# Performance work log

Hardware: AMD Instinct MI355X
Metric: run time of the kernel (lower is better)

Reference implementation:

```python
import jax, jax.numpy as jnp
import numpy as np

N_NODES = 100000
N_EDGES = 1600000
N_GRAPHS = 1024
IN_FEATS = 74
HID = 100


def setup_inputs() -> dict:
    key = jax.random.key(0)
    ks = jax.random.split(key, 16)
    node_feats = jax.random.normal(ks[0], (N_NODES, IN_FEATS), dtype=jnp.float32)
    src = jax.random.randint(ks[1], (N_EDGES,), 0, N_NODES, dtype=jnp.int32)
    dst = jax.random.randint(ks[2], (N_EDGES,), 0, N_NODES, dtype=jnp.int32)
    graph_ids = jnp.sort(jax.random.randint(ks[3], (N_NODES,), 0, N_GRAPHS, dtype=jnp.int32))

    def lin(k, fi, fo):
        s = 1.0 / np.sqrt(fi)
        kw, kb = jax.random.split(k)
        return (jax.random.uniform(kw, (fi, fo), jnp.float32, -s, s),
                jax.random.uniform(kb, (fo,), jnp.float32, -s, s))

    W_self1, _ = lin(ks[4], IN_FEATS, HID)
    W_neigh1, b1 = lin(ks[5], IN_FEATS, HID)
    W_self2, _ = lin(ks[6], HID, HID)
    W_neigh2, b2 = lin(ks[7], HID, HID)
    w_atom, b_atom = lin(ks[8], HID, 1)
    W_p1, b_p1 = lin(ks[9], 2 * HID, 64)
    W_p2, b_p2 = lin(ks[10], 64, 1)
    return {
        'node_feats': node_feats, 'src': src, 'dst': dst, 'graph_ids': graph_ids,
        'n_graphs': N_GRAPHS,
        'W_self1': W_self1, 'W_neigh1': W_neigh1, 'b1': b1,
        'W_self2': W_self2, 'W_neigh2': W_neigh2, 'b2': b2,
        'w_atom': w_atom, 'b_atom': b_atom,
        'W_p1': W_p1, 'b_p1': b_p1, 'W_p2': W_p2, 'b_p2': b_p2,
    }


def _sage_mean_layer(h, src, dst, W_self, W_neigh, b):
    # DGL SAGEConv, aggregator 'mean': out = h @ W_self + mean_{u->v}(h_u) @ W_neigh + b
    n = h.shape[0]
    msg = h[src]  # [E, F] gather
    agg = jax.ops.segment_sum(msg, dst, num_segments=n)
    deg = jax.ops.segment_sum(jnp.ones((src.shape[0],), h.dtype), dst, num_segments=n)
    h_neigh = agg / jnp.maximum(deg, 1.0)[:, None]
    return jax.nn.relu(h @ W_self + h_neigh @ W_neigh + b)


def reference(node_feats, src, dst, graph_ids, n_graphs,
              W_self1, W_neigh1, b1, W_self2, W_neigh2, b2,
              w_atom, b_atom, W_p1, b_p1, W_p2, b_p2):
    h = _sage_mean_layer(node_feats, src, dst, W_self1, W_neigh1, b1)
    h = _sage_mean_layer(h, src, dst, W_self2, W_neigh2, b2)

    # WeightedSumAndMax readout
    w = jax.nn.sigmoid(h @ w_atom + b_atom)          # [N, 1]
    g_sum = jax.ops.segment_sum(h * w, graph_ids, num_segments=n_graphs)   # [G, HID]
    g_max = jax.ops.segment_max(h, graph_ids, num_segments=n_graphs)       # [G, HID]
    g_max = jnp.where(jnp.isneginf(g_max), 0.0, g_max)  # empty graphs -> 0
    g_feats = jnp.concatenate([g_sum, g_max], axis=-1)  # [G, 2*HID]

    # MLP predictor: Linear(200,64) -> Linear(64,1) (no activation between)
    out = (g_feats @ W_p1 + b_p1) @ W_p2 + b_p2
    return out
```

## Files before the change

kernel.cpp:

```cpp
#include <hip/hip_runtime.h>

#define N_NODES 100000
#define N_PAD   100096
#define N_EDGES 1600000
#define N_GRAPHS 1024
#define F_IN 74
#define HID 100

#define KP1 160
#define KP2 224

#define FBF_LD 80
#define F8T_LD 80
#define AGT_LD 80
#define AGT2_LD 112
#define H1C8_LD 128
#define H2_LD  100

#define ZROW N_NODES

#define NB ((N_NODES + 255) / 256)
#define BKCAP 8192
#define BIN_EPB 4096
#define NBB ((N_EDGES + BIN_EPB - 1) / BIN_EPB)

typedef __attribute__((ext_vector_type(8))) short short8;
typedef __attribute__((ext_vector_type(4))) float f32x4;
typedef __attribute__((ext_vector_type(2))) float f32x2;

#if defined(__has_builtin)
#if __has_builtin(__builtin_amdgcn_cvt_pk_f32_fp8) && __has_builtin(__builtin_amdgcn_cvt_pk_fp8_f32)
#define HAVE_FP8 1
#endif
#endif

__device__ __forceinline__ unsigned short f2bf(float x) {
    union { float f; unsigned u; } c; c.f = x;
    unsigned u = c.u;
    unsigned r = (u + 0x7fffu + ((u >> 16) & 1u)) >> 16;
    return (unsigned short)r;
}
__device__ __forceinline__ float bf2f(unsigned short h) {
    union { unsigned u; float f; } c; c.u = ((unsigned)h) << 16;
    return c.f;
}
__device__ __forceinline__ float blo(unsigned w) { return bf2f((unsigned short)(w & 0xffffu)); }
__device__ __forceinline__ float bhi(unsigned w) { return bf2f((unsigned short)(w >> 16)); }
__device__ __forceinline__ unsigned bpack(float a, float b) {
    return (unsigned)f2bf(a) | ((unsigned)f2bf(b) << 16);
}
__device__ __forceinline__ void store8(void* p, unsigned lo, unsigned hi) {
    unsigned long long v = (unsigned long long)lo | ((unsigned long long)hi << 32);
    *(unsigned long long*)p = v;
}

__device__ __forceinline__ unsigned char enc_fp8_1(float v) {
#ifdef HAVE_FP8
    return (unsigned char)__builtin_amdgcn_cvt_pk_fp8_f32(v, 0.f, 0, false);
#else
    unsigned sgn = v < 0.f ? 0x80u : 0u;
    float m = fabsf(v);
    unsigned char mag;
    if (m < 0.015625f) {
        int q = (int)(m * 512.0f + 0.5f);
        mag = (unsigned char)(q > 7 ? 7 : q);
    } else {
        union { float f; unsigned u; } c; c.f = m;
        unsigned r = c.u + 0x7ffff + ((c.u >> 20) & 1u);
        int e = (int)(r >> 23) - 127;
        mag = (e > 8) ? (unsigned char)0x7e : (unsigned char)(((e + 7) << 3) | ((r >> 20) & 7u));
    }
    return (unsigned char)(sgn | mag);
#endif
}
__device__ __forceinline__ unsigned enc_fp8x4(float v0, float v1, float v2, float v3) {
#ifdef HAVE_FP8
    int r = __builtin_amdgcn_cvt_pk_fp8_f32(v0, v1, 0, false);
    r = __builtin_amdgcn_cvt_pk_fp8_f32(v2, v3, r, true);
    return (unsigned)r;
#else
    return (unsigned)enc_fp8_1(v0) | ((unsigned)enc_fp8_1(v1) << 8) |
           ((unsigned)enc_fp8_1(v2) << 16) | ((unsigned)enc_fp8_1(v3) << 24);
#endif
}
__device__ __forceinline__ void dec_fp8x4(unsigned w, float& x0, float& x1, float& x2, float& x3) {
#ifdef HAVE_FP8
    f32x2 lo = __builtin_amdgcn_cvt_pk_f32_fp8((int)w, false);
    f32x2 hi = __builtin_amdgcn_cvt_pk_f32_fp8((int)w, true);
    x0 = lo.x; x1 = lo.y; x2 = hi.x; x3 = hi.y;
#else
    auto d1 = [](unsigned b) -> float {
        float s = (b & 0x80u) ? -1.f : 1.f;
        b &= 0x7fu;
        if (b < 8) return s * (float)b * 0.001953125f;
        union { unsigned u; float f; } c;
        c.u = ((((b >> 3) & 15u) - 7 + 127) << 23) | ((b & 7u) << 20);
        return s * c.f;
    };
    x0 = d1(w & 0xffu); x1 = d1((w >> 8) & 0xffu);
    x2 = d1((w >> 16) & 0xffu); x3 = d1(w >> 24);
#endif
}
__device__ __forceinline__ short8 dec8bf(uint2 v) {
    float x0, x1, x2, x3, y0, y1, y2, y3;
    dec_fp8x4(v.x, x0, x1, x2, x3);
    dec_fp8x4(v.y, y0, y1, y2, y3);
    union { short8 s; unsigned u[4]; } r;
    r.u[0] = bpack(x0, x1); r.u[1] = bpack(x2, x3);
    r.u[2] = bpack(y0, y1); r.u[3] = bpack(y2, y3);
    return r.s;
}


__global__ __launch_bounds__(256) void k_bin(const int* __restrict__ src,
                                             const int* __restrict__ dst,
                                             int* __restrict__ bucket_fill,
                                             unsigned* __restrict__ bbuf) {
    __shared__ int cnt[NB];
    __shared__ int base[NB];
    int t = threadIdx.x;
    for (int i = t; i < NB; i += 256) cnt[i] = 0;
    __syncthreads();
    int e0 = blockIdx.x * BIN_EPB;
    int e1 = e0 + BIN_EPB < N_EDGES ? e0 + BIN_EPB : N_EDGES;
    for (int e = e0 + t; e < e1; e += 256) {
        atomicAdd(&cnt[dst[e] >> 8], 1);
    }
    __syncthreads();
    for (int i = t; i < NB; i += 256) {
        int c = cnt[i];
        base[i] = c ? atomicAdd(&bucket_fill[i], c) : 0;
        cnt[i] = 0;
    }
    __syncthreads();
    for (int e = e0 + t; e < e1; e += 256) {
        int d = dst[e];
        int b = d >> 8;
        int pos = atomicAdd(&cnt[b], 1);
        bbuf[(size_t)b * BKCAP + base[b] + pos] = ((unsigned)src[e] << 8) | (unsigned)(d & 255);
    }
}

__global__ __launch_bounds__(256) void k_scatter(const unsigned* __restrict__ bbuf,
                                                 const int* __restrict__ bucket_fill,
                                                 int2* __restrict__ rp2,
                                                 int* __restrict__ csr) {
    __shared__ int fc[256];
    __shared__ int ofs[256];
    __shared__ int wsum[4];
    int b = blockIdx.x, t = threadIdx.x;
    int nstart = b << 8;
    int base = b * BKCAP;
    int bend = base + bucket_fill[b];
    fc[t] = 0;
    __syncthreads();
    for (int i = base + t; i < bend; i += 256)
        atomicAdd(&fc[bbuf[i] & 255u], 1);
    __syncthreads();
    int d = fc[t];
    int dp = (d + 7) & ~7;
    int lane = t & 63, w = t >> 6;
    int inc = dp;
    #pragma unroll
    for (int o = 1; o < 64; o <<= 1) {
        int x = __shfl_up(inc, o, 64);
        if (lane >= o) inc += x;
    }
    if (lane == 63) wsum[w] = inc;
    __syncthreads();
    int woff = 0;
    for (int i = 0; i < w; ++i) woff += wsum[i];
    ofs[t] = base + woff + inc - dp;
    __syncthreads();
    int node = nstart + t;
    int o0 = ofs[t];
    if (node < N_NODES) rp2[node] = make_int2(o0, o0 + d);
    for (int i = o0 + d; i < o0 + dp; ++i) csr[i] = ZROW;
    fc[t] = 0;
    __syncthreads();
    for (int i = base + t; i < bend; i += 256) {
        unsigned p = bbuf[i];
        int dl = (int)(p & 255u);
        int pos = atomicAdd(&fc[dl], 1);
        csr[ofs[dl] + pos] = (int)(p >> 8);
    }
}


__global__ void k_feats(const float* __restrict__ feats, short* __restrict__ fbf,
                        unsigned* __restrict__ f8t, unsigned* __restrict__ h1c8) {
    int idx = blockIdx.x * blockDim.x + threadIdx.x;
    if (idx < H1C8_LD / 4) h1c8[(size_t)ZROW * (H1C8_LD / 4) + idx] = 0u;
    if (idx >= (N_NODES + 1) * (F8T_LD / 4)) return;
    int n = idx / (F8T_LD / 4), g = idx - n * (F8T_LD / 4);
    int c0 = 4 * g;
    float v0 = 0.f, v1 = 0.f, v2 = 0.f, v3 = 0.f;
    if (n < N_NODES) {
        const float* r = feats + (size_t)n * F_IN;
        v0 = (c0 + 0 < F_IN) ? r[c0 + 0] : 0.f;
        v1 = (c0 + 1 < F_IN) ? r[c0 + 1] : 0.f;
        v2 = (c0 + 2 < F_IN) ? r[c0 + 2] : 0.f;
        v3 = (c0 + 3 < F_IN) ? r[c0 + 3] : 0.f;
    }
    unsigned* fb = (unsigned*)fbf + (size_t)n * (FBF_LD / 2) + 2 * g;
    fb[0] = bpack(v0, v1);
    fb[1] = bpack(v2, v3);
    f8t[idx] = enc_fp8x4(v0, v1, v2, v3);
}


template <int KP, int K1, int AGG0>
__global__ void k_wconv(const float* __restrict__ Ws, const float* __restrict__ Wn,
                        short* __restrict__ Whi, short* __restrict__ Wlo) {
    int idx = blockIdx.x * blockDim.x + threadIdx.x;
    if (idx >= 112 * KP) return;
    int col = idx / KP, k = idx - col * KP;
    float v = 0.f;
    if (col < HID) {
        if (k < K1) v = Ws[k * HID + col];
        else if (k >= AGG0 && k < AGG0 + K1) v = Wn[(k - AGG0) * HID + col];
    }
    unsigned short hi = f2bf(v);
    unsigned short lo = f2bf(v - bf2f(hi));
    Whi[idx] = (short)hi;
    Wlo[idx] = (short)lo;
}


__global__ __launch_bounds__(256) void k_prep1(const unsigned char* __restrict__ f8t,
                        const int2* __restrict__ rp2, const int* __restrict__ csr,
                        short* __restrict__ agt) {
    int wid = threadIdx.x >> 6, lane = threadIdx.x & 63;
    int v = blockIdx.x * 4 + wid;
    if (v >= N_NODES) return;
    int h = lane >> 5, q = lane & 31;
    int2 se = rp2[v];
    int s = se.x, e = se.y;
    int deg = e - s;
    int pe = s + ((deg + 7) & ~7);
    float a0 = 0.f, a1 = 0.f, a2 = 0.f, a3 = 0.f;
    if (q < 19) {
        #pragma unroll 2
        for (int j = s; j < pe; j += 8) {
            unsigned w0 = *(const unsigned*)(f8t + (size_t)csr[j + h] * F8T_LD + q * 4);
            unsigned w1 = *(const unsigned*)(f8t + (size_t)csr[j + 2 + h] * F8T_LD + q * 4);
            unsigned w2 = *(const unsigned*)(f8t + (size_t)csr[j + 4 + h] * F8T_LD + q * 4);
            unsigned w3 = *(const unsigned*)(f8t + (size_t)csr[j + 6 + h] * F8T_LD + q * 4);
            float x0, x1, x2, x3;
            dec_fp8x4(w0, x0, x1, x2, x3); a0 += x0; a1 += x1; a2 += x2; a3 += x3;
            dec_fp8x4(w1, x0, x1, x2, x3); a0 += x0; a1 += x1; a2 += x2; a3 += x3;
            dec_fp8x4(w2, x0, x1, x2, x3); a0 += x0; a1 += x1; a2 += x2; a3 += x3;
            dec_fp8x4(w3, x0, x1, x2, x3); a0 += x0; a1 += x1; a2 += x2; a3 += x3;
        }
    }
    a0 += __shfl_xor(a0, 32, 64);
    a1 += __shfl_xor(a1, 32, 64);
    a2 += __shfl_xor(a2, 32, 64);
    a3 += __shfl_xor(a3, 32, 64);
    float inv = 1.0f / fmaxf((float)deg, 1.0f);
    if (h == 0 && q < 20) {
        store8((char*)agt + (size_t)v * (AGT_LD * 2) + q * 8,
               bpack(a0 * inv, a1 * inv), bpack(a2 * inv, a3 * inv));
    }
}


__global__ __launch_bounds__(256) void k_prep2(const unsigned char* __restrict__ h1c8,
                        const int2* __restrict__ rp2, const int* __restrict__ csr,
                        short* __restrict__ agt2) {
    int wid = threadIdx.x >> 6, lane = threadIdx.x & 63;
    int v = blockIdx.x * 4 + wid;
    if (v >= N_NODES) return;
    int h = lane >> 5, q = lane & 31;
    int2 se = rp2[v];
    int s = se.x, e = se.y;
    int deg = e - s;
    int pe = s + ((deg + 7) & ~7);
    float a0 = 0.f, a1 = 0.f, a2 = 0.f, a3 = 0.f;
    if (q < 25) {
        #pragma unroll 2
        for (int j = s; j < pe; j += 8) {
            unsigned w0 = *(const unsigned*)(h1c8 + (size_t)csr[j + h] * H1C8_LD + q * 4);
            unsigned w1 = *(const unsigned*)(h1c8 + (size_t)csr[j + 2 + h] * H1C8_LD + q * 4);
            unsigned w2 = *(const unsigned*)(h1c8 + (size_t)csr[j + 4 + h] * H1C8_LD + q * 4);
            unsigned w3 = *(const unsigned*)(h1c8 + (size_t)csr[j + 6 + h] * H1C8_LD + q * 4);
            float x0, x1, x2, x3;
            dec_fp8x4(w0, x0, x1, x2, x3); a0 += x0; a1 += x1; a2 += x2; a3 += x3;
            dec_fp8x4(w1, x0, x1, x2, x3); a0 += x0; a1 += x1; a2 += x2; a3 += x3;
            dec_fp8x4(w2, x0, x1, x2, x3); a0 += x0; a1 += x1; a2 += x2; a3 += x3;
            dec_fp8x4(w3, x0, x1, x2, x3); a0 += x0; a1 += x1; a2 += x2; a3 += x3;
        }
    }
    a0 += __shfl_xor(a0, 32, 64);
    a1 += __shfl_xor(a1, 32, 64);
    a2 += __shfl_xor(a2, 32, 64);
    a3 += __shfl_xor(a3, 32, 64);
    float inv = 1.0f / fmaxf((float)deg, 1.0f);
    char* Aw = (char*)agt2 + (size_t)v * (AGT2_LD * 2);
    if (h == 0 && q < 25) {
        store8(Aw + q * 8, bpack(a0 * inv, a1 * inv), bpack(a2 * inv, a3 * inv));
    }
    if (h == 1 && q < 3) {
        store8(Aw + 200 + q * 8, 0u, 0u);
    }
}


__global__ __launch_bounds__(256) void k_mfma1(
    const short* __restrict__ fbf, const short* __restrict__ agt,
    const short* __restrict__ Wthi, const short* __restrict__ Wtlo,
    const float* __restrict__ bias, unsigned char* __restrict__ h1c8) {
    int t = threadIdx.x;
    int wid = t >> 6, lane = t & 63;
    int quad = lane >> 4, lr = lane & 15;
    int rowbase = blockIdx.x * 128 + wid * 32;

    short8 ap[2][5];
    #pragma unroll
    for (int rf = 0; rf < 2; ++rf) {
        int row = rowbase + rf * 16 + lr;
        #pragma unroll
        for (int c = 0; c < 5; ++c) {
            const short* p;
            if (c < 2) p = fbf + (size_t)row * FBF_LD + c * 32 + quad * 8;
            else if (c == 2) p = (quad < 2) ? fbf + (size_t)row * FBF_LD + 64 + quad * 8
                                            : agt + (size_t)row * AGT_LD + (quad - 2) * 8;
            else p = agt + (size_t)row * AGT_LD + (c - 3) * 32 + 16 + quad * 8;
            ap[rf][c] = *(const short8*)p;
        }
    }

    f32x4 acc[2][7];
    #pragma unroll
    for (int rf = 0; rf < 2; ++rf)
        #pragma unroll
        for (int n = 0; n < 7; ++n) acc[rf][n] = (f32x4){0.f, 0.f, 0.f, 0.f};

    #pragma unroll
    for (int c = 0; c < 5; ++c) {
        #pragma unroll
        for (int n = 0; n < 7; ++n) {
            size_t off = (size_t)(n * 16 + lr) * KP1 + c * 32 + quad * 8;
            short8 wh = *(const short8*)(Wthi + off);
            short8 wl = *(const short8*)(Wtlo + off);
            #pragma unroll
            for (int rf = 0; rf < 2; ++rf) {
                acc[rf][n] = __builtin_amdgcn_mfma_f32_16x16x32_bf16(ap[rf][c], wh, acc[rf][n], 0, 0, 0);
                acc[rf][n] = __builtin_amdgcn_mfma_f32_16x16x32_bf16(ap[rf][c], wl, acc[rf][n], 0, 0, 0);
            }
        }
    }

    #pragma unroll
    for (int rf = 0; rf < 2; ++rf) {
        #pragma unroll
        for (int n = 0; n < 7; ++n) {
            int col = n * 16 + lr;
            float bv = (col < HID) ? bias[col] : 0.f;
            #pragma unroll
            for (int r = 0; r < 4; ++r) {
                int row = rowbase + rf * 16 + quad * 4 + r;
                if (row < N_NODES) {
                    unsigned char enc = 0;
                    if (col < HID) enc = enc_fp8_1(fmaxf(acc[rf][n][r] + bv, 0.f));
                    h1c8[(size_t)row * H1C8_LD + col] = enc;
                }
            }
        }
        #pragma unroll
        for (int r = 0; r < 4; ++r) {
            int row = rowbase + rf * 16 + quad * 4 + r;
            if (row < N_NODES) h1c8[(size_t)row * H1C8_LD + 112 + lr] = 0;
        }
    }
}


__global__ __launch_bounds__(256) void k_mfma2(
    const unsigned char* __restrict__ h1c8, const short* __restrict__ agt2,
    const short* __restrict__ Wthi, const short* __restrict__ Wtlo,
    const float* __restrict__ bias, short* __restrict__ h2c) {
    int t = threadIdx.x;
    int wid = t >> 6, lane = t & 63;
    int quad = lane >> 4, lr = lane & 15;
    int rowbase = blockIdx.x * 128 + wid * 32;

    short8 ap[2][7];
    #pragma unroll
    for (int rf = 0; rf < 2; ++rf) {
        int row = rowbase + rf * 16 + lr;
        const unsigned char* hr = h1c8 + (size_t)row * H1C8_LD;
        const short* ar = agt2 + (size_t)row * AGT2_LD;
        #pragma unroll
        for (int c = 0; c < 7; ++c) {
            if (c < 3) {
                ap[rf][c] = dec8bf(*(const uint2*)(hr + c * 32 + quad * 8));
            } else if (c == 3) {
                if (quad < 2) ap[rf][c] = dec8bf(*(const uint2*)(hr + 96 + quad * 8));
                else ap[rf][c] = *(const short8*)(ar + (quad - 2) * 8);
            } else {
                ap[rf][c] = *(const short8*)(ar + (c - 4) * 32 + 16 + quad * 8);
            }
        }
    }

    f32x4 acc[2][7];
    #pragma unroll
    for (int rf = 0; rf < 2; ++rf)
        #pragma unroll
        for (int n = 0; n < 7; ++n) acc[rf][n] = (f32x4){0.f, 0.f, 0.f, 0.f};

    #pragma unroll
    for (int c = 0; c < 7; ++c) {
        #pragma unroll
        for (int n = 0; n < 7; ++n) {
            size_t off = (size_t)(n * 16 + lr) * KP2 + c * 32 + quad * 8;
            short8 wh = *(const short8*)(Wthi + off);
            short8 wl = *(const short8*)(Wtlo + off);
            #pragma unroll
            for (int rf = 0; rf < 2; ++rf) {
                acc[rf][n] = __builtin_amdgcn_mfma_f32_16x16x32_bf16(ap[rf][c], wh, acc[rf][n], 0, 0, 0);
                acc[rf][n] = __builtin_amdgcn_mfma_f32_16x16x32_bf16(ap[rf][c], wl, acc[rf][n], 0, 0, 0);
            }
        }
    }

    #pragma unroll
    for (int rf = 0; rf < 2; ++rf) {
        #pragma unroll
        for (int n = 0; n < 7; ++n) {
            int col = n * 16 + lr;
            if (col < HID) {
                float bv = bias[col];
                #pragma unroll
                for (int r = 0; r < 4; ++r) {
                    int row = rowbase + rf * 16 + quad * 4 + r;
                    if (row < N_NODES) {
                        float v = fmaxf(acc[rf][n][r] + bv, 0.f);
                        h2c[(size_t)row * H2_LD + col] = (short)f2bf(v);
                    }
                }
            }
        }
    }
}


__global__ __launch_bounds__(256) void k_atomw(
    const unsigned short* __restrict__ h2c, const float* __restrict__ w_atom,
    const float* __restrict__ b_atom, float* __restrict__ aw) {
    int t = threadIdx.x;
    int hw = t >> 5, q = t & 31;
    int row = blockIdx.x * 8 + hw;
    if (row >= N_NODES) return;
    float dot = 0.f;
    if (q < 25) {
        uint2 v = *(const uint2*)(h2c + (size_t)row * H2_LD + q * 4);
        float4 wa = *(const float4*)&w_atom[q * 4];
        dot = blo(v.x) * wa.x + bhi(v.x) * wa.y + blo(v.y) * wa.z + bhi(v.y) * wa.w;
    }
    #pragma unroll
    for (int off = 16; off; off >>= 1) dot += __shfl_xor(dot, off, 32);
    if (q == 0) aw[row] = 1.f / (1.f + __expf(-(dot + b_atom[0])));
}


__global__ void k_weff(const float* __restrict__ Wp1, const float* __restrict__ bp1,
                       const float* __restrict__ Wp2, const float* __restrict__ bp2,
                       float* __restrict__ weff) {
    int t = threadIdx.x;
    if (t < 200) {
        float s = 0.f;
        for (int k = 0; k < 64; ++k) s += Wp1[t * 64 + k] * Wp2[k];
        weff[t] = s;
    } else if (t == 200) {
        float s = bp2[0];
        for (int k = 0; k < 64; ++k) s += bp1[k] * Wp2[k];
        weff[200] = s;
    }
}


__global__ __launch_bounds__(256) void k_readout(
    const unsigned short* __restrict__ h2c, const float* __restrict__ aw,
    const int* __restrict__ graph_ids, const float* __restrict__ weff,
    float* __restrict__ out) {
    int g = blockIdx.x;
    int t = threadIdx.x, lane = t & 63, w = t >> 6;

    int s_, e_;
    {
        int l = 0, r = N_NODES;
        while (l < r) { int m = (l + r) >> 1; if (graph_ids[m] < g) l = m + 1; else r = m; }
        s_ = l;
        l = s_; r = N_NODES;
        while (l < r) { int m = (l + r) >> 1; if (graph_ids[m] < g + 1) l = m + 1; else r = m; }
        e_ = l;
    }

    float sum0 = 0.f, sum1 = 0.f, mx0 = 0.f, mx1 = 0.f;
    for (int i = s_ + w; i < e_; i += 4) {
        float wt = aw[i];
        if (lane < 50) {
            unsigned wv = *(const unsigned*)(h2c + (size_t)i * H2_LD + 2 * lane);
            float v0 = blo(wv), v1 = bhi(wv);
            sum0 += v0 * wt;
            sum1 += v1 * wt;
            mx0 = fmaxf(mx0, v0);
            mx1 = fmaxf(mx1, v1);
        }
    }

    __shared__ float ssum[4][HID];
    __shared__ float smx[4][HID];
    if (lane < 50) {
        ssum[w][2 * lane] = sum0;
        ssum[w][2 * lane + 1] = sum1;
        smx[w][2 * lane] = mx0;
        smx[w][2 * lane + 1] = mx1;
    }
    __syncthreads();

    float contrib = 0.f;
    if (t < HID) {
        float sumf = ssum[0][t] + ssum[1][t] + ssum[2][t] + ssum[3][t];
        float mxf = fmaxf(fmaxf(smx[0][t], smx[1][t]), fmaxf(smx[2][t], smx[3][t]));
        contrib = sumf * weff[t] + mxf * weff[HID + t];
    }
    #pragma unroll
    for (int off = 32; off; off >>= 1) contrib += __shfl_xor(contrib, off, 64);
    __shared__ float red[4];
    if (lane == 0) red[w] = contrib;
    __syncthreads();
    if (t == 0) out[g] = red[0] + red[1] + red[2] + red[3] + weff[200];
}


extern "C" void kernel_launch(void* const* d_in, const int* in_sizes, int n_in,
                              void* d_out, int out_size, void* d_ws, size_t ws_size,
                              hipStream_t stream) {
    const float* node_feats = (const float*)d_in[0];
    const int* src = (const int*)d_in[1];
    const int* dst = (const int*)d_in[2];
    const int* gid = (const int*)d_in[3];
    const float* Ws1 = (const float*)d_in[5];
    const float* Wn1 = (const float*)d_in[6];
    const float* b1 = (const float*)d_in[7];
    const float* Ws2 = (const float*)d_in[8];
    const float* Wn2 = (const float*)d_in[9];
    const float* b2 = (const float*)d_in[10];
    const float* w_atom = (const float*)d_in[11];
    const float* b_atom = (const float*)d_in[12];
    const float* Wp1 = (const float*)d_in[13];
    const float* bp1 = (const float*)d_in[14];
    const float* Wp2 = (const float*)d_in[15];
    const float* bp2 = (const float*)d_in[16];
    float* out = (float*)d_out;

    char* ws = (char*)d_ws;
    size_t off = 0;
    auto alloc = [&](size_t bytes) -> void* {
        void* p = (void*)(ws + off);
        off += (bytes + 255) & ~(size_t)255;
        return p;
    };
    int2* rp2 = (int2*)alloc((size_t)N_NODES * sizeof(int2));
    int* bucket_fill = (int*)alloc(NB * sizeof(int));
    int* csr = (int*)alloc((size_t)NB * BKCAP * sizeof(int));
    unsigned* bbuf = (unsigned*)alloc((size_t)NB * BKCAP * sizeof(unsigned));
    short* fbf = (short*)alloc((size_t)(N_PAD + 1) * FBF_LD * sizeof(short));
    unsigned char* f8t = (unsigned char*)alloc((size_t)(N_PAD + 1) * F8T_LD);
    short* agt = (short*)alloc((size_t)N_PAD * AGT_LD * sizeof(short));
    short* agt2 = (short*)alloc((size_t)N_PAD * AGT2_LD * sizeof(short));
    unsigned char* h1c8 = (unsigned char*)alloc((size_t)(N_NODES + 1) * H1C8_LD);
    short* h2c = (short*)alloc((size_t)N_NODES * H2_LD * sizeof(short));
    float* aw = (float*)alloc((size_t)N_NODES * sizeof(float));
    short* Wt1hi = (short*)alloc(112 * KP1 * sizeof(short));
    short* Wt1lo = (short*)alloc(112 * KP1 * sizeof(short));
    short* Wt2hi = (short*)alloc(112 * KP2 * sizeof(short));
    short* Wt2lo = (short*)alloc(112 * KP2 * sizeof(short));
    float* weff = (float*)alloc(256 * sizeof(float));

    hipMemsetAsync(bucket_fill, 0, NB * sizeof(int), stream);

    k_bin<<<NBB, 256, 0, stream>>>(src, dst, bucket_fill, bbuf);
    k_scatter<<<NB, 256, 0, stream>>>(bbuf, bucket_fill, rp2, csr);

    k_feats<<<((N_NODES + 1) * (F8T_LD / 4) + 255) / 256, 256, 0, stream>>>(
        node_feats, fbf, (unsigned*)f8t, (unsigned*)h1c8);
    k_wconv<KP1, F_IN, 80><<<(112 * KP1 + 255) / 256, 256, 0, stream>>>(Ws1, Wn1, Wt1hi, Wt1lo);
    k_wconv<KP2, HID, 112><<<(112 * KP2 + 255) / 256, 256, 0, stream>>>(Ws2, Wn2, Wt2hi, Wt2lo);

    k_prep1<<<(N_NODES + 3) / 4, 256, 0, stream>>>(f8t, rp2, csr, agt);
    k_mfma1<<<N_PAD / 128, 256, 0, stream>>>(fbf, agt, Wt1hi, Wt1lo, b1, h1c8);
    k_prep2<<<(N_NODES + 3) / 4, 256, 0, stream>>>(h1c8, rp2, csr, agt2);
    k_mfma2<<<N_PAD / 128, 256, 0, stream>>>(h1c8, agt2, Wt2hi, Wt2lo, b2, h2c);

    k_atomw<<<(N_NODES + 7) / 8, 256, 0, stream>>>((const unsigned short*)h2c, w_atom, b_atom, aw);
    k_weff<<<1, 256, 0, stream>>>(Wp1, bp1, Wp2, bp2, weff);
    k_readout<<<N_GRAPHS, 256, 0, stream>>>((const unsigned short*)h2c, aw, gid, weff, out);
}
```

Baseline: 256.6 us.

## Stage MFMA weights in LDS and split output columns across two blocks

```diff
diff --git a/kernel.cpp b/kernel.cpp
--- a/kernel.cpp
+++ b/kernel.cpp
@@ -9,6 +9,9 @@
 
 #define KP1 160
 #define KP2 224
+
+#define PAD1 168
+#define PAD2 232
 
 #define FBF_LD 80
 #define F8T_LD 80
@@ -310,10 +313,26 @@
     const short* __restrict__ fbf, const short* __restrict__ agt,
     const short* __restrict__ Wthi, const short* __restrict__ Wtlo,
     const float* __restrict__ bias, unsigned char* __restrict__ h1c8) {
+    __shared__ short Wlds[2][64 * PAD1];
     int t = threadIdx.x;
+    int nh = blockIdx.x & 1, rb = blockIdx.x >> 1;
+    const int NG = nh ? 3 : 4;
+    const int ng0 = nh ? 4 : 0;
+    {
+        const unsigned* gh = (const unsigned*)(Wthi + (size_t)(ng0 * 16) * KP1);
+        const unsigned* gl = (const unsigned*)(Wtlo + (size_t)(ng0 * 16) * KP1);
+        unsigned* lh = (unsigned*)&Wlds[0][0];
+        unsigned* ll = (unsigned*)&Wlds[1][0];
+        int tot = NG * 16 * (KP1 / 2);
+        for (int i = t; i < tot; i += 256) {
+            int row = i / (KP1 / 2), cu = i - row * (KP1 / 2);
+            lh[row * (PAD1 / 2) + cu] = gh[i];
+            ll[row * (PAD1 / 2) + cu] = gl[i];
+        }
+    }
     int wid = t >> 6, lane = t & 63;
     int quad = lane >> 4, lr = lane & 15;
-    int rowbase = blockIdx.x * 128 + wid * 32;
+    int rowbase = rb * 128 + wid * 32;
 
     short8 ap[2][5];
     #pragma unroll
@@ -329,24 +348,27 @@
             ap[rf][c] = *(const short8*)p;
         }
     }
-
-    f32x4 acc[2][7];
+    __syncthreads();
+
+    f32x4 acc[2][4];
     #pragma unroll
     for (int rf = 0; rf < 2; ++rf)
         #pragma unroll
-        for (int n = 0; n < 7; ++n) acc[rf][n] = (f32x4){0.f, 0.f, 0.f, 0.f};
+        for (int n = 0; n < 4; ++n) acc[rf][n] = (f32x4){0.f, 0.f, 0.f, 0.f};
 
     #pragma unroll
     for (int c = 0; c < 5; ++c) {
         #pragma unroll
-        for (int n = 0; n < 7; ++n) {
-            size_t off = (size_t)(n * 16 + lr) * KP1 + c * 32 + quad * 8;
-            short8 wh = *(const short8*)(Wthi + off);
-            short8 wl = *(const short8*)(Wtlo + off);
-            #pragma unroll
-            for (int rf = 0; rf < 2; ++rf) {
-                acc[rf][n] = __builtin_amdgcn_mfma_f32_16x16x32_bf16(ap[rf][c], wh, acc[rf][n], 0, 0, 0);
-                acc[rf][n] = __builtin_amdgcn_mfma_f32_16x16x32_bf16(ap[rf][c], wl, acc[rf][n], 0, 0, 0);
+        for (int n = 0; n < 4; ++n) {
+            if (n < NG) {
+                int loff = (n * 16 + lr) * PAD1 + c * 32 + quad * 8;
+                short8 wh = *(const short8*)&Wlds[0][loff];
+                short8 wl = *(const short8*)&Wlds[1][loff];
+                #pragma unroll
+                for (int rf = 0; rf < 2; ++rf) {
+                    acc[rf][n] = __builtin_amdgcn_mfma_f32_16x16x32_bf16(ap[rf][c], wh, acc[rf][n], 0, 0, 0);
+                    acc[rf][n] = __builtin_amdgcn_mfma_f32_16x16x32_bf16(ap[rf][c], wl, acc[rf][n], 0, 0, 0);
+                }
             }
         }
     }
@@ -354,23 +376,27 @@
     #pragma unroll
     for (int rf = 0; rf < 2; ++rf) {
         #pragma unroll
-        for (int n = 0; n < 7; ++n) {
-            int col = n * 16 + lr;
-            float bv = (col < HID) ? bias[col] : 0.f;
+        for (int n = 0; n < 4; ++n) {
+            if (n < NG) {
+                int col = ng0 * 16 + n * 16 + lr;
+                float bv = (col < HID) ? bias[col] : 0.f;
+                #pragma unroll
+                for (int r = 0; r < 4; ++r) {
+                    int row = rowbase + rf * 16 + quad * 4 + r;
+                    if (row < N_NODES) {
+                        unsigned char enc = 0;
+                        if (col < HID) enc = enc_fp8_1(fmaxf(acc[rf][n][r] + bv, 0.f));
+                        h1c8[(size_t)row * H1C8_LD + col] = enc;
+                    }
+                }
+            }
+        }
+        if (nh == 1) {
             #pragma unroll
             for (int r = 0; r < 4; ++r) {
                 int row = rowbase + rf * 16 + quad * 4 + r;
-                if (row < N_NODES) {
-                    unsigned char enc = 0;
-                    if (col < HID) enc = enc_fp8_1(fmaxf(acc[rf][n][r] + bv, 0.f));
-                    h1c8[(size_t)row * H1C8_LD + col] = enc;
-                }
+                if (row < N_NODES) h1c8[(size_t)row * H1C8_LD + 112 + lr] = 0;
             }
-        }
-        #pragma unroll
-        for (int r = 0; r < 4; ++r) {
-            int row = rowbase + rf * 16 + quad * 4 + r;
-            if (row < N_NODES) h1c8[(size_t)row * H1C8_LD + 112 + lr] = 0;
         }
     }
 }
@@ -380,10 +406,26 @@
     const unsigned char* __restrict__ h1c8, const short* __restrict__ agt2,
     const short* __restrict__ Wthi, const short* __restrict__ Wtlo,
     const float* __restrict__ bias, short* __restrict__ h2c) {
+    __shared__ short Wlds[2][64 * PAD2];
     int t = threadIdx.x;
+    int nh = blockIdx.x & 1, rb = blockIdx.x >> 1;
+    const int NG = nh ? 3 : 4;
+    const int ng0 = nh ? 4 : 0;
+    {
+        const unsigned* gh = (const unsigned*)(Wthi + (size_t)(ng0 * 16) * KP2);
+        const unsigned* gl = (const unsigned*)(Wtlo + (size_t)(ng0 * 16) * KP2);
+        unsigned* lh = (unsigned*)&Wlds[0][0];
+        unsigned* ll = (unsigned*)&Wlds[1][0];
+        int tot = NG * 16 * (KP2 / 2);
+        for (int i = t; i < tot; i += 256) {
+            int row = i / (KP2 / 2), cu = i - row * (KP2 / 2);
+            lh[row * (PAD2 / 2) + cu] = gh[i];
+            ll[row * (PAD2 / 2) + cu] = gl[i];
+        }
+    }
     int wid = t >> 6, lane = t & 63;
     int quad = lane >> 4, lr = lane & 15;
-    int rowbase = blockIdx.x * 128 + wid * 32;
+    int rowbase = rb * 128 + wid * 32;
 
     short8 ap[2][7];
     #pragma unroll
@@ -403,24 +445,27 @@
             }
         }
     }
-
-    f32x4 acc[2][7];
+    __syncthreads();
+
+    f32x4 acc[2][4];
     #pragma unroll
     for (int rf = 0; rf < 2; ++rf)
         #pragma unroll
-        for (int n = 0; n < 7; ++n) acc[rf][n] = (f32x4){0.f, 0.f, 0.f, 0.f};
+        for (int n = 0; n < 4; ++n) acc[rf][n] = (f32x4){0.f, 0.f, 0.f, 0.f};
 
     #pragma unroll
     for (int c = 0; c < 7; ++c) {
         #pragma unroll
-        for (int n = 0; n < 7; ++n) {
-            size_t off = (size_t)(n * 16 + lr) * KP2 + c * 32 + quad * 8;
-            short8 wh = *(const short8*)(Wthi + off);
-            short8 wl = *(const short8*)(Wtlo + off);
-            #pragma unroll
-            for (int rf = 0; rf < 2; ++rf) {
-                acc[rf][n] = __builtin_amdgcn_mfma_f32_16x16x32_bf16(ap[rf][c], wh, acc[rf][n], 0, 0, 0);
-                acc[rf][n] = __builtin_amdgcn_mfma_f32_16x16x32_bf16(ap[rf][c], wl, acc[rf][n], 0, 0, 0);
+        for (int n = 0; n < 4; ++n) {
+            if (n < NG) {
+                int loff = (n * 16 + lr) * PAD2 + c * 32 + quad * 8;
+                short8 wh = *(const short8*)&Wlds[0][loff];
+                short8 wl = *(const short8*)&Wlds[1][loff];
+                #pragma unroll
+                for (int rf = 0; rf < 2; ++rf) {
+                    acc[rf][n] = __builtin_amdgcn_mfma_f32_16x16x32_bf16(ap[rf][c], wh, acc[rf][n], 0, 0, 0);
+                    acc[rf][n] = __builtin_amdgcn_mfma_f32_16x16x32_bf16(ap[rf][c], wl, acc[rf][n], 0, 0, 0);
+                }
             }
         }
     }
@@ -428,16 +473,18 @@
     #pragma unroll
     for (int rf = 0; rf < 2; ++rf) {
         #pragma unroll
-        for (int n = 0; n < 7; ++n) {
-            int col = n * 16 + lr;
-            if (col < HID) {
-                float bv = bias[col];
-                #pragma unroll
-                for (int r = 0; r < 4; ++r) {
-                    int row = rowbase + rf * 16 + quad * 4 + r;
-                    if (row < N_NODES) {
-                        float v = fmaxf(acc[rf][n][r] + bv, 0.f);
-                        h2c[(size_t)row * H2_LD + col] = (short)f2bf(v);
+        for (int n = 0; n < 4; ++n) {
+            if (n < NG) {
+                int col = ng0 * 16 + n * 16 + lr;
+                if (col < HID) {
+                    float bv = bias[col];
+                    #pragma unroll
+                    for (int r = 0; r < 4; ++r) {
+                        int row = rowbase + rf * 16 + quad * 4 + r;
+                        if (row < N_NODES) {
+                            float v = fmaxf(acc[rf][n][r] + bv, 0.f);
+                            h2c[(size_t)row * H2_LD + col] = (short)f2bf(v);
+                        }
                     }
                 }
             }
@@ -592,9 +639,9 @@
     k_wconv<KP2, HID, 112><<<(112 * KP2 + 255) / 256, 256, 0, stream>>>(Ws2, Wn2, Wt2hi, Wt2lo);
 
     k_prep1<<<(N_NODES + 3) / 4, 256, 0, stream>>>(f8t, rp2, csr, agt);
-    k_mfma1<<<N_PAD / 128, 256, 0, stream>>>(fbf, agt, Wt1hi, Wt1lo, b1, h1c8);
+    k_mfma1<<<(N_PAD / 128) * 2, 256, 0, stream>>>(fbf, agt, Wt1hi, Wt1lo, b1, h1c8);
     k_prep2<<<(N_NODES + 3) / 4, 256, 0, stream>>>(h1c8, rp2, csr, agt2);
-    k_mfma2<<<N_PAD / 128, 256, 0, stream>>>(h1c8, agt2, Wt2hi, Wt2lo, b2, h2c);
+    k_mfma2<<<(N_PAD / 128) * 2, 256, 0, stream>>>(h1c8, agt2, Wt2hi, Wt2lo, b2, h2c);
 
     k_atomw<<<(N_NODES + 7) / 8, 256, 0, stream>>>((const unsigned short*)h2c, w_atom, b_atom, aw);
     k_weff<<<1, 256, 0, stream>>>(Wp1, bp1, Wp2, bp2, weff);
```

Result: slower. 267.5 us (+4.2%).
